# Optimization experiments

Hardware: AMD Instinct MI355X
Metric: run time of the kernel (lower is better)

Reference implementation:

```python
import jax, jax.numpy as jnp
import numpy as np

PI = float(np.pi)
LN_EPS = 1e-5
COS_EPS = 1e-6

D_HIDDEN, N_HEADS, D_HEAD, D_MLP = 1024, 16, 64, 4096
B, T = 4, 2048


def _xavier(key, shape):
    # torch xavier_uniform on 3D tensor: fan_in = shape[1]*shape[2]? torch uses
    # fan_in = shape[1] * receptive_field(shape[2:]), fan_out = shape[0] * rf.
    rf = 1
    for s in shape[2:]:
        rf *= s
    fan_in, fan_out = shape[1] * rf, shape[0] * rf
    bound = float(np.sqrt(6.0 / (fan_in + fan_out)))
    return jax.random.uniform(key, shape, jnp.float32, -bound, bound)


def setup_inputs() -> dict:
    key = jax.random.key(0)
    ks = jax.random.split(key, 10)
    x = jax.random.normal(ks[0], (B, T, D_HIDDEN), jnp.float32)
    W_Q = _xavier(ks[1], (N_HEADS, D_HIDDEN, 1))
    W_K = _xavier(ks[2], (N_HEADS, D_HIDDEN, 1))
    W_V = _xavier(ks[3], (N_HEADS, D_HIDDEN, D_HEAD))
    W_O = _xavier(ks[4], (D_HIDDEN, D_HEAD, N_HEADS))
    ln1_w = jnp.ones((D_HIDDEN,), jnp.float32)
    ln1_b = jnp.zeros((D_HIDDEN,), jnp.float32)
    ln2_w = jnp.ones((D_HIDDEN,), jnp.float32)
    ln2_b = jnp.zeros((D_HIDDEN,), jnp.float32)
    s1 = 1.0 / np.sqrt(D_HIDDEN)
    s2 = 1.0 / np.sqrt(D_MLP)
    W1 = jax.random.uniform(ks[5], (D_HIDDEN, D_MLP), jnp.float32, -s1, s1)
    b1 = jax.random.uniform(ks[6], (D_MLP,), jnp.float32, -s1, s1)
    W2 = jax.random.uniform(ks[7], (D_MLP, D_HIDDEN), jnp.float32, -s2, s2)
    b2 = jax.random.uniform(ks[8], (D_HIDDEN,), jnp.float32, -s2, s2)
    return {"x": x, "W_Q": W_Q, "W_K": W_K, "W_V": W_V, "W_O": W_O,
            "ln1_w": ln1_w, "ln1_b": ln1_b, "ln2_w": ln2_w, "ln2_b": ln2_b,
            "W1": W1, "b1": b1, "W2": W2, "b2": b2}


def _layer_norm(x, w, b):
    mu = jnp.mean(x, axis=-1, keepdims=True)
    var = jnp.mean(jnp.square(x - mu), axis=-1, keepdims=True)
    return (x - mu) * jax.lax.rsqrt(var + LN_EPS) * w + b


def _cos_attention(y, W_Q, W_K, W_V, W_O):
    q = jnp.einsum('btd,idh->btih', y, W_Q)  # (B,T,H,1)
    k = jnp.einsum('btd,idh->btih', y, W_K)  # (B,T,H,1)
    V = jnp.einsum('btd,idh->btih', y, W_V)  # (B,T,H,Dh)
    # use_tanh branch
    q = jnp.tanh(q) * (PI / 4)
    k = jnp.tanh(k) * (PI / 4)
    cos_k, sin_k = jnp.cos(k), jnp.sin(k)
    cos_KV = jnp.cumsum(cos_k * V, axis=1)
    sin_KV = jnp.cumsum(sin_k * V, axis=1)
    cos_Q, sin_Q = jnp.cos(q), jnp.sin(q)
    heads = cos_Q * cos_KV + sin_Q * sin_KV  # (B,T,H,Dh)
    # epsilon branch: normalizing denominator
    cos_K = jnp.cumsum(cos_k, axis=1)
    sin_K = jnp.cumsum(sin_k, axis=1)
    denom = cos_Q * cos_K + sin_Q * sin_K + COS_EPS  # (B,T,H,1)
    heads = heads / denom
    return jnp.einsum('dhi,btih->btd', W_O, heads)


def reference(x, W_Q, W_K, W_V, W_O, ln1_w, ln1_b, ln2_w, ln2_b, W1, b1, W2, b2):
    y = _layer_norm(x, ln1_w, ln1_b)
    x = x + _cos_attention(y, W_Q, W_K, W_V, W_O)
    y = _layer_norm(x, ln2_w, ln2_b)
    mlp = jnp.dot(jax.nn.gelu(jnp.dot(y, W1) + b1), W2) + b2
    return x + mlp
```

## Files before the change

### kernel.cpp

```cpp
#include <hip/hip_runtime.h>
#include <hip/hip_bf16.h>
#include <stdint.h>

typedef unsigned short u16;
typedef __attribute__((ext_vector_type(4))) unsigned int u32x4;
typedef __attribute__((ext_vector_type(8))) __bf16 bfx8;
typedef __attribute__((ext_vector_type(4))) float f32x4;

#define PI_F 3.14159265358979323846f

__device__ __forceinline__ float bf2f(u16 u) {
    unsigned v = ((unsigned)u) << 16; float f; __builtin_memcpy(&f, &v, 4); return f;
}
__device__ __forceinline__ u16 f2bf(float f) {
    unsigned u; __builtin_memcpy(&u, &f, 4);
    unsigned r = (u + 0x7fffu + ((u >> 16) & 1u)) >> 16; return (u16)r;
}

__global__ __launch_bounds__(256)
void tconv_kernel(const float* __restrict__ in, u16* __restrict__ out,
                  int R, int C, long inBatch, long outBatch)
{
    __shared__ float tile[64][65];
    const int tx = threadIdx.x & 63;
    const int ty = threadIdx.x >> 6;
    const int bc = blockIdx.x * 64;
    const int br = blockIdx.y * 64;
    const float* ip = in + (long)blockIdx.z * inBatch;
    u16* op = out + (long)blockIdx.z * outBatch;

    #pragma unroll
    for (int rr = ty; rr < 64; rr += 4) {
        int r = br + rr, c = bc + tx;
        tile[rr][tx] = (r < R && c < C) ? ip[(long)r * C + c] : 0.f;
    }
    __syncthreads();
    #pragma unroll
    for (int rr = ty; rr < 64; rr += 4) {
        int oc = bc + rr;
        int orr = br + tx;
        if (oc < C && orr < R)
            op[(long)oc * R + orr] = f2bf(tile[tx][rr]);
    }
}

template<bool DO_QK>
__global__ __launch_bounds__(256)
void ln_kernel(const float* __restrict__ X, const float* __restrict__ w,
               const float* __restrict__ b, u16* __restrict__ Ybf,
               const float* __restrict__ WQ, const float* __restrict__ WK,
               float* __restrict__ cqA, float* __restrict__ sqA,
               float* __restrict__ ckA, float* __restrict__ skA)
{
    __shared__ float yrow[1024];
    __shared__ float wsum[4], wsq[4];
    const int row = blockIdx.x;
    const int tid = threadIdx.x;
    const int lane = tid & 63;
    const int wv = tid >> 6;

    const float4 xv = ((const float4*)(X + (long)row * 1024))[tid];
    float s  = xv.x + xv.y + xv.z + xv.w;
    float sq = xv.x*xv.x + xv.y*xv.y + xv.z*xv.z + xv.w*xv.w;
    #pragma unroll
    for (int off = 32; off; off >>= 1) {
        s  += __shfl_down(s, off);
        sq += __shfl_down(sq, off);
    }
    if (lane == 0) { wsum[wv] = s; wsq[wv] = sq; }
    __syncthreads();
    const float ts = wsum[0] + wsum[1] + wsum[2] + wsum[3];
    const float tq = wsq[0] + wsq[1] + wsq[2] + wsq[3];
    const float mean = ts * (1.f / 1024.f);
    const float var  = tq * (1.f / 1024.f) - mean * mean;
    const float rstd = rsqrtf(var + 1e-5f);

    const float4 wv4 = ((const float4*)w)[tid];
    const float4 bv4 = ((const float4*)b)[tid];
    const float y0 = (xv.x - mean) * rstd * wv4.x + bv4.x;
    const float y1 = (xv.y - mean) * rstd * wv4.y + bv4.y;
    const float y2 = (xv.z - mean) * rstd * wv4.z + bv4.z;
    const float y3 = (xv.w - mean) * rstd * wv4.w + bv4.w;

    uint2 p;
    p.x = (unsigned)f2bf(y0) | ((unsigned)f2bf(y1) << 16);
    p.y = (unsigned)f2bf(y2) | ((unsigned)f2bf(y3) << 16);
    ((uint2*)(Ybf + (long)row * 1024))[tid] = p;

    if (DO_QK) {
        yrow[tid*4+0] = y0; yrow[tid*4+1] = y1;
        yrow[tid*4+2] = y2; yrow[tid*4+3] = y3;
        __syncthreads();
        #pragma unroll
        for (int i = 0; i < 4; ++i) {
            const int h = wv * 4 + i;
            const float* wqp = WQ + (long)h * 1024;
            const float* wkp = WK + (long)h * 1024;
            float dq = 0.f, dk = 0.f;
            #pragma unroll
            for (int j = 0; j < 16; ++j) {
                const float yv = yrow[lane + 64*j];
                dq = fmaf(yv, wqp[lane + 64*j], dq);
                dk = fmaf(yv, wkp[lane + 64*j], dk);
            }
            #pragma unroll
            for (int off = 32; off; off >>= 1) {
                dq += __shfl_down(dq, off);
                dk += __shfl_down(dk, off);
            }
            if (lane == 0) {
                const float aq = tanhf(dq) * (PI_F * 0.25f);
                const float ak = tanhf(dk) * (PI_F * 0.25f);
                float sv, cv;
                const long o = (long)h * 8192 + row;
                __sincosf(aq, &sv, &cv); cqA[o] = cv; sqA[o] = sv;
                __sincosf(ak, &sv, &cv); ckA[o] = cv; skA[o] = sv;
            }
        }
    }
}

__global__ __launch_bounds__(64)
void scan_kernel(const u16* __restrict__ V,
                 const float* __restrict__ cqA, const float* __restrict__ sqA,
                 const float* __restrict__ ckA, const float* __restrict__ skA,
                 u16* __restrict__ H)
{
    __shared__ u16 vt[64][64];
    __shared__ float lck[64], lsk[64], lrc[64], lrs[64];
    const int b = blockIdx.x >> 4;
    const int h = blockIdx.x & 15;
    const int lane = threadIdx.x;
    const long rowbase = (long)b * 2048;
    const long colbase = (long)h * 64;
    const long qbase = (long)h * 8192 + rowbase;

    float csum = 0.f, ssum = 0.f;
    float carry_c = 0.f, carry_s = 0.f;

    for (int ch = 0; ch < 32; ++ch) {
        const int t0 = ch * 64;
        __syncthreads();
        #pragma unroll
        for (int i = 0; i < 8; ++i) {
            const int tt = i * 8 + (lane >> 3);
            const int c0 = (lane & 7) * 8;
            *(u32x4*)&vt[tt][c0] =
                *(const u32x4*)(V + (rowbase + t0 + tt) * 1024 + colbase + c0);
        }
        {
            const float ck = ckA[qbase + t0 + lane];
            const float sk = skA[qbase + t0 + lane];
            const float cq = cqA[qbase + t0 + lane];
            const float sq = sqA[qbase + t0 + lane];
            float c = ck, sscan = sk;
            #pragma unroll
            for (int off = 1; off < 64; off <<= 1) {
                const float oc = __shfl_up(c, off);
                const float os = __shfl_up(sscan, off);
                if (lane >= off) { c += oc; sscan += os; }
            }
            const float cK = carry_c + c;
            const float sK = carry_s + sscan;
            carry_c += __shfl(c, 63);
            carry_s += __shfl(sscan, 63);
            const float denom = cq * cK + sq * sK + 1e-6f;
            lck[lane] = ck; lsk[lane] = sk;
            lrc[lane] = cq / denom; lrs[lane] = sq / denom;
        }
        __syncthreads();
        u16* outp = H + (rowbase + t0) * 1024 + colbase + lane;
        #pragma unroll 8
        for (int tt = 0; tt < 64; ++tt) {
            const float v = bf2f(vt[tt][lane]);
            csum = fmaf(lck[tt], v, csum);
            ssum = fmaf(lsk[tt], v, ssum);
            const float hv = lrc[tt] * csum + lrs[tt] * ssum;
            outp[(long)tt * 1024] = f2bf(hv);
        }
    }
}

template<int EPI>
__global__ __launch_bounds__(256, 2)
void gemm_bt(const u16* __restrict__ A, const u16* __restrict__ B,
             void* __restrict__ Cout, const float* __restrict__ res,
             const float* __restrict__ bias, int M, int N, int K)
{
    __shared__ u16 As[128 * 32];
    __shared__ u16 Bs[128 * 32];
    const int tid  = threadIdx.x;
    const int lane = tid & 63;
    const int wave = tid >> 6;
    const int wr = wave >> 1;
    const int wc = wave & 1;
    const int brow = blockIdx.y * 128;
    const int bcol = blockIdx.x * 128;

    const int srow = tid >> 2;
    const int scol = (tid & 3) * 8;
    const u16* Ag = A + (long)(brow + srow) * K + scol;
    const u16* Bg = B + (long)(bcol + srow) * K + scol;

    f32x4 acc[4][4];
    #pragma unroll
    for (int i = 0; i < 4; ++i)
        #pragma unroll
        for (int j = 0; j < 4; ++j) acc[i][j] = (f32x4){0.f, 0.f, 0.f, 0.f};

    const int KT = K >> 5;
    u32x4 ar0 = *(const u32x4*)(Ag);
    u32x4 ar1 = *(const u32x4*)(Ag + (long)64 * K);
    u32x4 br0 = *(const u32x4*)(Bg);
    u32x4 br1 = *(const u32x4*)(Bg + (long)64 * K);

    const int kgrp = (lane >> 4) * 8;
    const int rr = lane & 15;

    for (int kt = 0; kt < KT; ++kt) {
        __syncthreads();
        *(u32x4*)&As[srow * 32 + scol]        = ar0;
        *(u32x4*)&As[(srow + 64) * 32 + scol] = ar1;
        *(u32x4*)&Bs[srow * 32 + scol]        = br0;
        *(u32x4*)&Bs[(srow + 64) * 32 + scol] = br1;
        __syncthreads();
        if (kt + 1 < KT) {
            const u16* Ag2 = Ag + (kt + 1) * 32;
            const u16* Bg2 = Bg + (kt + 1) * 32;
            ar0 = *(const u32x4*)(Ag2);
            ar1 = *(const u32x4*)(Ag2 + (long)64 * K);
            br0 = *(const u32x4*)(Bg2);
            br1 = *(const u32x4*)(Bg2 + (long)64 * K);
        }
        bfx8 af[4], bfr[4];
        #pragma unroll
        for (int m = 0; m < 4; ++m)
            af[m] = *(const bfx8*)&As[(wr * 64 + m * 16 + rr) * 32 + kgrp];
        #pragma unroll
        for (int n = 0; n < 4; ++n)
            bfr[n] = *(const bfx8*)&Bs[(wc * 64 + n * 16 + rr) * 32 + kgrp];
        #pragma unroll
        for (int m = 0; m < 4; ++m)
            #pragma unroll
            for (int n = 0; n < 4; ++n)
                acc[m][n] = __builtin_amdgcn_mfma_f32_16x16x32_bf16(
                    af[m], bfr[n], acc[m][n], 0, 0, 0);
    }

    const int crow0 = brow + wr * 64 + (lane >> 4) * 4;
    const int ccol0 = bcol + wc * 64 + (lane & 15);
    #pragma unroll
    for (int m = 0; m < 4; ++m) {
        #pragma unroll
        for (int n = 0; n < 4; ++n) {
            const int col = ccol0 + n * 16;
            #pragma unroll
            for (int r = 0; r < 4; ++r) {
                const int row = crow0 + m * 16 + r;
                const long idx = (long)row * N + col;
                const float v = acc[m][n][r];
                if (EPI == 0) {
                    ((u16*)Cout)[idx] = f2bf(v);
                } else if (EPI == 1) {
                    ((float*)Cout)[idx] = v + res[idx];
                } else if (EPI == 2) {
                    const float hh = v + bias[col];
                    const float g = 0.5f * hh *
                        (1.f + tanhf(0.7978845608028654f * (hh + 0.044715f * hh * hh * hh)));
                    ((u16*)Cout)[idx] = f2bf(g);
                } else {
                    ((float*)Cout)[idx] = v + res[idx] + bias[col];
                }
            }
        }
    }
}

extern "C" void kernel_launch(void* const* d_in, const int* in_sizes, int n_in,
                              void* d_out, int out_size, void* d_ws, size_t ws_size,
                              hipStream_t stream)
{
    (void)in_sizes; (void)n_in; (void)out_size; (void)ws_size;
    const float* x    = (const float*)d_in[0];
    const float* WQ   = (const float*)d_in[1];
    const float* WK   = (const float*)d_in[2];
    const float* WV   = (const float*)d_in[3];
    const float* WO   = (const float*)d_in[4];
    const float* ln1w = (const float*)d_in[5];
    const float* ln1b = (const float*)d_in[6];
    const float* ln2w = (const float*)d_in[7];
    const float* ln2b = (const float*)d_in[8];
    const float* W1   = (const float*)d_in[9];
    const float* b1   = (const float*)d_in[10];
    const float* W2   = (const float*)d_in[11];
    const float* b2   = (const float*)d_in[12];
    float* out = (float*)d_out;

    char* ws = (char*)d_ws;
    u16*   Ybf  = (u16*)(ws + 0);
    u16*   Vbf  = (u16*)(ws + 16777216);
    u16*   Hbf  = (u16*)(ws + 33554432);
    float* X2   = (float*)(ws + 50331648);
    u16*   H1   = (u16*)(ws + 83886080);
    u16*   WVT  = (u16*)(ws + 150994944);
    u16*   WOT  = (u16*)(ws + 153092096);
    u16*   W1T  = (u16*)(ws + 155189248);
    u16*   W2T  = (u16*)(ws + 163577856);
    float* CQ   = (float*)(ws + 171966464);
    float* SQ   = (float*)(ws + 172490752);
    float* CK   = (float*)(ws + 173015040);
    float* SK   = (float*)(ws + 173539328);

    tconv_kernel<<<dim3(1, 16, 16), 256, 0, stream>>>(WV, WVT, 1024, 64, 1024L*64, 64L*1024);
    tconv_kernel<<<dim3(1, 1, 1024), 256, 0, stream>>>(WO, WOT, 64, 16, 1024L, 1024L);
    tconv_kernel<<<dim3(64, 16, 1), 256, 0, stream>>>(W1, W1T, 1024, 4096, 0L, 0L);
    tconv_kernel<<<dim3(16, 64, 1), 256, 0, stream>>>(W2, W2T, 4096, 1024, 0L, 0L);

    ln_kernel<true><<<8192, 256, 0, stream>>>(x, ln1w, ln1b, Ybf, WQ, WK, CQ, SQ, CK, SK);

    gemm_bt<0><<<dim3(8, 64), 256, 0, stream>>>(Ybf, WVT, Vbf, nullptr, nullptr, 8192, 1024, 1024);

    scan_kernel<<<64, 64, 0, stream>>>(Vbf, CQ, SQ, CK, SK, Hbf);

    gemm_bt<1><<<dim3(8, 64), 256, 0, stream>>>(Hbf, WOT, X2, x, nullptr, 8192, 1024, 1024);

    ln_kernel<false><<<8192, 256, 0, stream>>>(X2, ln2w, ln2b, Ybf,
                                               nullptr, nullptr, nullptr, nullptr, nullptr, nullptr);

    gemm_bt<2><<<dim3(32, 64), 256, 0, stream>>>(Ybf, W1T, H1, nullptr, b1, 8192, 4096, 1024);

    gemm_bt<3><<<dim3(8, 64), 256, 0, stream>>>(H1, W2T, out, X2, b2, 8192, 1024, 4096);
}
```

Measured before the change: 560.8 us.

## Load GEMM tiles directly into LDS with a swizzled layout

Replaces the register-staged global-to-LDS copies in the bf16 GEMM with global_load_lds direct-to-LDS transfers. Each thread's source chunk is rotated by row, and the fragment reads use the matching swizzled offsets, to reduce LDS bank conflicts. This removes the VGPR round trip and the LDS store instructions. In exchange it drops the register prefetch of the next k-tile: loads are now issued and waited on inside the same iteration, so latency is hidden only across the two resident blocks per CU.

```diff
diff --git a/kernel.cpp b/kernel.cpp
--- a/kernel.cpp
+++ b/kernel.cpp
@@ -15,6 +15,13 @@
 __device__ __forceinline__ u16 f2bf(float f) {
     unsigned u; __builtin_memcpy(&u, &f, 4);
     unsigned r = (u + 0x7fffu + ((u >> 16) & 1u)) >> 16; return (u16)r;
+}
+
+__device__ __forceinline__ void glds16(const u16* g, const u16* l) {
+    __builtin_amdgcn_global_load_lds(
+        (const __attribute__((address_space(1))) unsigned int*)(unsigned long long)g,
+        (__attribute__((address_space(3))) unsigned int*)(unsigned int)(unsigned long long)l,
+        16, 0, 0);
 }
 
 __global__ __launch_bounds__(256)
@@ -198,9 +205,14 @@
     const int bcol = blockIdx.x * 128;
 
     const int srow = tid >> 2;
-    const int scol = (tid & 3) * 8;
-    const u16* Ag = A + (long)(brow + srow) * K + scol;
-    const u16* Bg = B + (long)(bcol + srow) * K + scol;
+    const int cdst = tid & 3;
+    const int csrc = (cdst - (srow >> 1)) & 3;
+    const u16* Ag = A + (long)(brow + srow) * K + csrc * 8;
+    const u16* Bg = B + (long)(bcol + srow) * K + csrc * 8;
+    const u16* lA0 = &As[tid * 8];
+    const u16* lA1 = &As[2048 + tid * 8];
+    const u16* lB0 = &Bs[tid * 8];
+    const u16* lB1 = &Bs[2048 + tid * 8];
 
     f32x4 acc[4][4];
     #pragma unroll
@@ -208,37 +220,29 @@
         #pragma unroll
         for (int j = 0; j < 4; ++j) acc[i][j] = (f32x4){0.f, 0.f, 0.f, 0.f};
 
+    const int rr = lane & 15;
+    const int physc = ((lane >> 4) + (rr >> 1)) & 3;
+    const char* Ab = (const char*)As;
+    const char* Bb = (const char*)Bs;
+    const int aoff0 = (wr * 64 + rr) * 64 + physc * 16;
+    const int boff0 = (wc * 64 + rr) * 64 + physc * 16;
+
     const int KT = K >> 5;
-    u32x4 ar0 = *(const u32x4*)(Ag);
-    u32x4 ar1 = *(const u32x4*)(Ag + (long)64 * K);
-    u32x4 br0 = *(const u32x4*)(Bg);
-    u32x4 br1 = *(const u32x4*)(Bg + (long)64 * K);
-
-    const int kgrp = (lane >> 4) * 8;
-    const int rr = lane & 15;
-
     for (int kt = 0; kt < KT; ++kt) {
-        __syncthreads();
-        *(u32x4*)&As[srow * 32 + scol]        = ar0;
-        *(u32x4*)&As[(srow + 64) * 32 + scol] = ar1;
-        *(u32x4*)&Bs[srow * 32 + scol]        = br0;
-        *(u32x4*)&Bs[(srow + 64) * 32 + scol] = br1;
-        __syncthreads();
-        if (kt + 1 < KT) {
-            const u16* Ag2 = Ag + (kt + 1) * 32;
-            const u16* Bg2 = Bg + (kt + 1) * 32;
-            ar0 = *(const u32x4*)(Ag2);
-            ar1 = *(const u32x4*)(Ag2 + (long)64 * K);
-            br0 = *(const u32x4*)(Bg2);
-            br1 = *(const u32x4*)(Bg2 + (long)64 * K);
-        }
+        const long ko = (long)kt * 32;
+        __syncthreads();
+        glds16(Ag + ko, lA0);
+        glds16(Ag + ko + (long)64 * K, lA1);
+        glds16(Bg + ko, lB0);
+        glds16(Bg + ko + (long)64 * K, lB1);
+        __syncthreads();
         bfx8 af[4], bfr[4];
         #pragma unroll
         for (int m = 0; m < 4; ++m)
-            af[m] = *(const bfx8*)&As[(wr * 64 + m * 16 + rr) * 32 + kgrp];
+            af[m] = *(const bfx8*)(Ab + aoff0 + m * (16 * 64));
         #pragma unroll
         for (int n = 0; n < 4; ++n)
-            bfr[n] = *(const bfx8*)&Bs[(wc * 64 + n * 16 + rr) * 32 + kgrp];
+            bfr[n] = *(const bfx8*)(Bb + boff0 + n * (16 * 64));
         #pragma unroll
         for (int m = 0; m < 4; ++m)
             #pragma unroll
```

Result: no change. 559.4 us (-0.2%).
